# Optimization experiments

Measured on AMD Instinct MI355X. Metric: run time of the kernel, lower is better.

The kernel has to match this reference:

```python
import jax, jax.numpy as jnp
import numpy as np

K = 31  # box-filter kernel size
PAD = 15

def _avg_pool_31(x):
    # count_include_pad=True (torch default): divide by K*K everywhere
    s = jax.lax.reduce_window(x, 0.0, jax.lax.add,
                              window_dimensions=(1, 1, K, K),
                              window_strides=(1, 1, 1, 1),
                              padding=((0, 0), (0, 0), (PAD, PAD), (PAD, PAD)))
    return s / (K * K)

def setup_inputs() -> dict:
    key = jax.random.key(0)
    k1, k2 = jax.random.split(key)
    pred = jax.random.normal(k1, (64, 1, 512, 512), dtype=jnp.float32)
    mask = jax.random.uniform(k2, (64, 1, 512, 512), dtype=jnp.float32)
    return {"pred": pred, "mask": mask}

def reference(pred, mask):
    weight = 1.0 + 5.0 * jnp.abs(_avg_pool_31(mask) - mask)
    # binary_cross_entropy_with_logits, reduction='none' (stable form)
    bce = jnp.maximum(pred, 0.0) - pred * mask + jnp.log1p(jnp.exp(-jnp.abs(pred)))
    p = jax.nn.sigmoid(pred)
    inter = p * mask
    union = p + mask
    iou = 1.0 - (inter + 1.0) / (union - inter + 1.0)
    wsum = weight.sum(axis=(2, 3))  # [B, C]
    weighted_bce = (weight * bce).sum(axis=(2, 3)) / wsum
    weighted_iou = (weight * iou).sum(axis=(2, 3)) / wsum
    return (weighted_bce + weighted_iou).mean()
```

## Files before the change

kernel.cpp:

```cpp
#include <hip/hip_runtime.h>
#include <math.h>

#define BATCH 64
#define H 512
#define W 512
#define KRAD 15
#define STRIP 64
#define NSTRIP (H / STRIP)
#define RING 40

__device__ __forceinline__ float wave_reduce(float v) {
    #pragma unroll
    for (int off = 32; off > 0; off >>= 1) v += __shfl_xor(v, off);
    return v;
}

__device__ __forceinline__ unsigned bf16b(float f) {
    unsigned u = __float_as_uint(f);
    return (u + 0x7FFFu + ((u >> 16) & 1u)) >> 16;
}
__device__ __forceinline__ float fbf16(unsigned short s) {
    return __uint_as_float(((unsigned)s) << 16);
}

__device__ __forceinline__ void scan_row(const float* __restrict__ img_base, int r,
                                         int lane, unsigned short* dst) {
    float o[8];
    if (0 <= r && r < H) {
        const float4* in4 = reinterpret_cast<const float4*>(img_base + (size_t)r * W + lane * 8);
        float4 va = in4[0], vb = in4[1];
        float v[8] = {va.x, va.y, va.z, va.w, vb.x, vb.y, vb.z, vb.w};
        float P[8];
        float run = 0.f;
        #pragma unroll
        for (int k = 0; k < 8; ++k) { run += v[k]; P[k] = run; }
        float scan = run;
        #pragma unroll
        for (int off = 1; off < 64; off <<= 1) {
            float n = __shfl_up(scan, off);
            if (lane >= off) scan += n;
        }
        const float excl = scan - run;
        #pragma unroll
        for (int k = 0; k < 8; ++k) P[k] += excl;
        const float total = __shfl(P[7], 63);
        float shA[8], shB[8];
        shA[0] = __shfl_down(P[7], 1);
        #pragma unroll
        for (int k = 1; k < 8; ++k) shA[k] = __shfl_down(P[k - 1], 2);
        #pragma unroll
        for (int k = 0; k < 8; ++k) shB[k] = __shfl_up(P[k], 2);
        const int xb = lane * 8;
        #pragma unroll
        for (int k = 0; k < 8; ++k) {
            const int x = xb + k;
            const float A  = (x + KRAD <= W - 1) ? shA[k] : total;
            const float Bv = (x >= KRAD + 1) ? shB[k] : 0.f;
            o[k] = A - Bv;
        }
    } else {
        #pragma unroll
        for (int k = 0; k < 8; ++k) o[k] = 0.f;
    }
    uint4 wv;
    wv.x = bf16b(o[0]) | (bf16b(o[1]) << 16);
    wv.y = bf16b(o[2]) | (bf16b(o[3]) << 16);
    wv.z = bf16b(o[4]) | (bf16b(o[5]) << 16);
    wv.w = bf16b(o[6]) | (bf16b(o[7]) << 16);
    *reinterpret_cast<uint4*>(dst + lane * 8) = wv;
}

__global__ __launch_bounds__(512) void fused_kernel(const float* __restrict__ pred,
                                                    const float* __restrict__ mask,
                                                    float2* __restrict__ partials) {
    __shared__ unsigned short ring[RING][W];

    const int tid  = threadIdx.x;
    const int wave = tid >> 6;
    const int lane = tid & 63;
    const int img   = blockIdx.x >> 3;
    const int strip = blockIdx.x & 7;
    const int r0 = strip * STRIP;
    const int c  = tid;
    const float* mk = mask + (size_t)img * (H * W);
    const float* pr = pred + (size_t)img * (H * W);

    #pragma unroll
    for (int gp = 0; gp < 4; ++gp) {
        const int idx = gp * 8 + wave;
        if (idx < 31) scan_row(mk, r0 - 16 + idx, lane, &ring[idx][0]);
    }
    __syncthreads();

    float vsum = 0.f;
    #pragma unroll
    for (int s = 1; s <= 30; ++s) vsum += fbf16(ring[s][c]);

    float s0 = 0.f, s1 = 0.f;
    const float inv_k2 = 1.0f / 961.0f;
    int sA = 31;
    int sB = 0;

    for (int g = 0; g < STRIP / 8; ++g) {
        const int ybase = r0 + 8 * g;
        {
            int slot = sA + wave;
            if (slot >= RING) slot -= RING;
            scan_row(mk, ybase + 15 + wave, lane, &ring[slot][0]);
        }
        __syncthreads();

        float addv[8], subv[8], m[8], p[8];
        #pragma unroll
        for (int i = 0; i < 8; ++i) {
            int slotA = sA + i;
            if (slotA >= RING) slotA -= RING;
            addv[i] = fbf16(ring[slotA][c]);
            subv[i] = fbf16(ring[sB + i][c]);
        }
        #pragma unroll
        for (int i = 0; i < 8; ++i) {
            const int y = ybase + i;
            m[i] = mk[(size_t)y * W + c];
            p[i] = pr[(size_t)y * W + c];
        }
        #pragma unroll
        for (int i = 0; i < 8; ++i) {
            vsum += addv[i] - subv[i];
            const float avg = vsum * inv_k2;
            const float w = 1.0f + 5.0f * fabsf(avg - m[i]);
            const float e = __expf(-fabsf(p[i]));
            const float softplus = __logf(1.0f + e);
            const float bce = fmaxf(p[i], 0.0f) - p[i] * m[i] + softplus;
            const float r1pe = __builtin_amdgcn_rcpf(1.0f + e);
            const float sig = (p[i] >= 0.0f) ? r1pe : e * r1pe;
            const float inter = sig * m[i];
            const float denom = sig + m[i] - inter + 1.0f;
            const float iou = 1.0f - (inter + 1.0f) * __builtin_amdgcn_rcpf(denom);
            s0 += w;
            s1 += w * (bce + iou);
        }
        sA += 8; if (sA >= RING) sA -= RING;
        sB += 8; if (sB >= RING) sB -= RING;
        __syncthreads();
    }

    s0 = wave_reduce(s0);
    s1 = wave_reduce(s1);
    float2* wacc = reinterpret_cast<float2*>(&ring[0][0]);
    if (lane == 0) wacc[wave] = make_float2(s0, s1);
    __syncthreads();
    if (tid == 0) {
        float a0 = 0.f, a1 = 0.f;
        #pragma unroll
        for (int i = 0; i < 8; ++i) { a0 += wacc[i].x; a1 += wacc[i].y; }
        partials[blockIdx.x] = make_float2(a0, a1);
    }
}

__global__ void finalize_kernel(const float2* __restrict__ partials,
                                float* __restrict__ out) {
    const int lane = threadIdx.x;
    float s0 = 0.f, s1 = 0.f;
    #pragma unroll
    for (int j = 0; j < NSTRIP; ++j) {
        const float2 pp = partials[lane * NSTRIP + j];
        s0 += pp.x; s1 += pp.y;
    }
    float q = s1 / s0;
    q = wave_reduce(q);
    if (lane == 0) out[0] = q * (1.0f / (float)BATCH);
}

extern "C" void kernel_launch(void* const* d_in, const int* in_sizes, int n_in,
                              void* d_out, int out_size, void* d_ws, size_t ws_size,
                              hipStream_t stream) {
    const float* pred = (const float*)d_in[0];
    const float* mask = (const float*)d_in[1];
    float2* partials = (float2*)d_ws;

    hipLaunchKernelGGL(fused_kernel, dim3(BATCH * NSTRIP), dim3(512), 0, stream,
                       pred, mask, partials);
    hipLaunchKernelGGL(finalize_kernel, dim3(1), dim3(64), 0, stream,
                       partials, (float*)d_out);
}
```

Baseline: 45.62 us.

## Halve strip height and issue global loads before row scan and barrier

Splits each image into 16 strips of 32 rows instead of 8 of 64, doubling the block count to 1024 for better occupancy and load balance across CUs. Separates the row load from the prefix-scan/store so that the next mask row and the per-pixel mask/pred values are fetched before the scan and the barrier, overlapping global memory latency with shuffle work. The cost is more halo recomputation: each strip still scans 31 halo rows, so the redundant scan work per output row roughly doubles. Register pressure also rises from holding the prefetched values across the barrier.

New measurement: 55.37 us. 21.4% more time.

```diff
diff --git a/kernel.cpp b/kernel.cpp
--- a/kernel.cpp
+++ b/kernel.cpp
@@ -5,7 +5,7 @@
 #define H 512
 #define W 512
 #define KRAD 15
-#define STRIP 64
+#define STRIP 32
 #define NSTRIP (H / STRIP)
 #define RING 40
 
@@ -23,51 +23,55 @@
     return __uint_as_float(((unsigned)s) << 16);
 }
 
-__device__ __forceinline__ void scan_row(const float* __restrict__ img_base, int r,
-                                         int lane, unsigned short* dst) {
+__device__ __forceinline__ void load_row(const float* __restrict__ base, int r, int lane,
+                                         float4& a, float4& b) {
+    if (0 <= r && r < H) {
+        const float4* p4 = reinterpret_cast<const float4*>(base + (size_t)r * W + lane * 8);
+        a = p4[0]; b = p4[1];
+    } else {
+        a = make_float4(0.f, 0.f, 0.f, 0.f);
+        b = a;
+    }
+}
+
+__device__ __forceinline__ void scan_store(float4 va, float4 vb, int lane,
+                                           unsigned short* dst) {
+    float v[8] = {va.x, va.y, va.z, va.w, vb.x, vb.y, vb.z, vb.w};
+    float P[8];
+    float run = 0.f;
+    #pragma unroll
+    for (int k = 0; k < 8; ++k) { run += v[k]; P[k] = run; }
+    float scan = run;
+    #pragma unroll
+    for (int off = 1; off < 64; off <<= 1) {
+        float n = __shfl_up(scan, off);
+        if (lane >= off) scan += n;
+    }
+    const float excl = scan - run;
+    #pragma unroll
+    for (int k = 0; k < 8; ++k) P[k] += excl;
+    const float total = __shfl(P[7], 63);
+    float shA[8], shB[8];
+    shA[0] = __shfl_down(P[7], 1);
+    #pragma unroll
+    for (int k = 1; k < 8; ++k) shA[k] = __shfl_down(P[k - 1], 2);
+    #pragma unroll
+    for (int k = 0; k < 8; ++k) shB[k] = __shfl_up(P[k], 2);
+    const int xb = lane * 8;
     float o[8];
-    if (0 <= r && r < H) {
-        const float4* in4 = reinterpret_cast<const float4*>(img_base + (size_t)r * W + lane * 8);
-        float4 va = in4[0], vb = in4[1];
-        float v[8] = {va.x, va.y, va.z, va.w, vb.x, vb.y, vb.z, vb.w};
-        float P[8];
-        float run = 0.f;
-        #pragma unroll
-        for (int k = 0; k < 8; ++k) { run += v[k]; P[k] = run; }
-        float scan = run;
-        #pragma unroll
-        for (int off = 1; off < 64; off <<= 1) {
-            float n = __shfl_up(scan, off);
-            if (lane >= off) scan += n;
-        }
-        const float excl = scan - run;
-        #pragma unroll
-        for (int k = 0; k < 8; ++k) P[k] += excl;
-        const float total = __shfl(P[7], 63);
-        float shA[8], shB[8];
-        shA[0] = __shfl_down(P[7], 1);
-        #pragma unroll
-        for (int k = 1; k < 8; ++k) shA[k] = __shfl_down(P[k - 1], 2);
-        #pragma unroll
-        for (int k = 0; k < 8; ++k) shB[k] = __shfl_up(P[k], 2);
-        const int xb = lane * 8;
-        #pragma unroll
-        for (int k = 0; k < 8; ++k) {
-            const int x = xb + k;
-            const float A  = (x + KRAD <= W - 1) ? shA[k] : total;
-            const float Bv = (x >= KRAD + 1) ? shB[k] : 0.f;
-            o[k] = A - Bv;
-        }
-    } else {
-        #pragma unroll
-        for (int k = 0; k < 8; ++k) o[k] = 0.f;
+    #pragma unroll
+    for (int k = 0; k < 8; ++k) {
+        const int x = xb + k;
+        const float A  = (x + KRAD <= W - 1) ? shA[k] : total;
+        const float Bv = (x >= KRAD + 1) ? shB[k] : 0.f;
+        o[k] = A - Bv;
     }
     uint4 wv;
     wv.x = bf16b(o[0]) | (bf16b(o[1]) << 16);
     wv.y = bf16b(o[2]) | (bf16b(o[3]) << 16);
     wv.z = bf16b(o[4]) | (bf16b(o[5]) << 16);
     wv.w = bf16b(o[6]) | (bf16b(o[7]) << 16);
-    *reinterpret_cast<uint4*>(dst + lane * 8) = wv;
+    *reinterpret_cast<uint4*>(dst + xb) = wv;
 }
 
 __global__ __launch_bounds__(512) void fused_kernel(const float* __restrict__ pred,
@@ -78,8 +82,8 @@
     const int tid  = threadIdx.x;
     const int wave = tid >> 6;
     const int lane = tid & 63;
-    const int img   = blockIdx.x >> 3;
-    const int strip = blockIdx.x & 7;
+    const int img   = blockIdx.x >> 4;
+    const int strip = blockIdx.x & 15;
     const int r0 = strip * STRIP;
     const int c  = tid;
     const float* mk = mask + (size_t)img * (H * W);
@@ -88,7 +92,11 @@
     #pragma unroll
     for (int gp = 0; gp < 4; ++gp) {
         const int idx = gp * 8 + wave;
-        if (idx < 31) scan_row(mk, r0 - 16 + idx, lane, &ring[idx][0]);
+        if (idx < 31) {
+            float4 la, lb;
+            load_row(mk, r0 - 16 + idx, lane, la, lb);
+            scan_store(la, lb, lane, &ring[idx][0]);
+        }
     }
     __syncthreads();
 
@@ -103,26 +111,31 @@
 
     for (int g = 0; g < STRIP / 8; ++g) {
         const int ybase = r0 + 8 * g;
+
+        float4 sa, sb;
+        load_row(mk, ybase + 15 + wave, lane, sa, sb);
+        float m[8], p[8];
+        #pragma unroll
+        for (int i = 0; i < 8; ++i) {
+            const int y = ybase + i;
+            m[i] = mk[(size_t)y * W + c];
+            p[i] = pr[(size_t)y * W + c];
+        }
+
         {
             int slot = sA + wave;
             if (slot >= RING) slot -= RING;
-            scan_row(mk, ybase + 15 + wave, lane, &ring[slot][0]);
+            scan_store(sa, sb, lane, &ring[slot][0]);
         }
         __syncthreads();
 
-        float addv[8], subv[8], m[8], p[8];
+        float addv[8], subv[8];
         #pragma unroll
         for (int i = 0; i < 8; ++i) {
             int slotA = sA + i;
             if (slotA >= RING) slotA -= RING;
             addv[i] = fbf16(ring[slotA][c]);
             subv[i] = fbf16(ring[sB + i][c]);
-        }
-        #pragma unroll
-        for (int i = 0; i < 8; ++i) {
-            const int y = ybase + i;
-            m[i] = mk[(size_t)y * W + c];
-            p[i] = pr[(size_t)y * W + c];
         }
         #pragma unroll
         for (int i = 0; i < 8; ++i) {
```
